# Optimization experiments

Measured on AMD Instinct MI355X. Metric: run time of the kernel, lower is better.

The kernel has to match this reference:

```python
import jax, jax.numpy as jnp
import numpy as np

C, G = 128, 2000          # num_cells, total_genes
CE, GE, H = 64, 64, 256   # cell_embed_dim, gene_embed_dim, hidden_dim
F = CE + GE + 3           # FCGNN input: ctrl val + cell_embed + gene_embed + shift + num_cells


def setup_inputs() -> dict:
    key = jax.random.key(0)
    ks = jax.random.split(key, 13)
    s = 0.02
    return {
        "ctrl": jax.random.uniform(ks[0], (C, G), dtype=jnp.float32),
        "shift_vec": jax.random.normal(ks[1], (G,), dtype=jnp.float32),
        "gene_indices": jnp.arange(G, dtype=jnp.int32),
        # CellEmbedding params
        "ce_w1": jax.random.normal(ks[2], (G, H), dtype=jnp.float32) * s,
        "ce_b1": jnp.zeros((H,), dtype=jnp.float32),
        "ce_w2": jax.random.normal(ks[3], (H, CE), dtype=jnp.float32) * s,
        "ce_b2": jnp.zeros((CE,), dtype=jnp.float32),
        # gene embedding table
        "gene_table": jax.random.normal(ks[4], (G, GE), dtype=jnp.float32) * s,
        # FCGNN params
        "g_w1": jax.random.normal(ks[5], (F, H), dtype=jnp.float32) * s,
        "g_b1": jnp.zeros((H,), dtype=jnp.float32),
        "g_w2": jax.random.normal(ks[6], (2 * H, H), dtype=jnp.float32) * s,
        "g_b2": jnp.zeros((H,), dtype=jnp.float32),
        "g_w3": jax.random.normal(ks[7], (2 * H, 1), dtype=jnp.float32) * s,
        "g_b3": jnp.zeros((1,), dtype=jnp.float32),
    }


def reference(ctrl, shift_vec, gene_indices, ce_w1, ce_b1, ce_w2, ce_b2,
              gene_table, g_w1, g_b1, g_w2, g_b2, g_w3, g_b3):
    num_cells = ctrl.shape[0]
    num_genes = gene_indices.shape[0]

    # CellEmbedding: fc2(elu(fc1(ctrl)))  -> [C, CE]
    ce = jax.nn.elu(ctrl @ ce_w1 + ce_b1) @ ce_w2 + ce_b2

    ctrl_g = ctrl[:, gene_indices]           # [C, Gn]
    shift = shift_vec[gene_indices]          # [Gn]
    ge = gene_table[gene_indices]            # [Gn, GE]

    # Build [C, Gn, F] feature tensor (ctrl val, cell embed, gene embed, shift, num_cells)
    z = jnp.concatenate([
        ctrl_g[:, :, None],
        jnp.broadcast_to(ce[:, None, :], (num_cells, num_genes, ce.shape[1])),
        jnp.broadcast_to(ge[None, :, :], (num_cells, num_genes, ge.shape[1])),
        jnp.broadcast_to(shift[None, :, None], (num_cells, num_genes, 1)),
        jnp.full((num_cells, num_genes, 1), float(num_cells), dtype=ctrl.dtype),
    ], axis=2)

    # FCGNN applied per gene (vectorized over gene axis); pooling is mean over cells (axis 0)
    x = jax.nn.elu(z @ g_w1 + g_b1)                                   # [C, Gn, H]
    p = x.mean(axis=0)                                                # [Gn, H]
    x = jnp.concatenate([x, jnp.broadcast_to(p[None], x.shape)], -1) @ g_w2 + g_b2
    p = x.mean(axis=0)
    x = jax.nn.elu(jnp.concatenate([x, jnp.broadcast_to(p[None], x.shape)], -1)) @ g_w3 + g_b3
    out = x[..., 0]                                                   # [C, Gn]

    # softmax over cells (torch Softmax(dim=0) after transpose/squeeze)
    return jax.nn.softmax(out, axis=0)
```

## Files before the change

### kernel.cpp

```cpp
#include <hip/hip_runtime.h>
#include <hip/hip_bf16.h>
#include <math.h>

#define G_GENES 2000
#define C_CELLS 128
#define H_DIM   256
#define CE_DIM  64
#define LDAe    260

typedef __attribute__((ext_vector_type(8))) short short8;
typedef __attribute__((ext_vector_type(4))) float floatx4;

__device__ __forceinline__ float eluf(float x) {
    float e = __expf(x) - 1.0f;
    return x > 0.0f ? x : e;
}
__device__ __forceinline__ unsigned short f2bf(float v) {
    unsigned u = __float_as_uint(v);
    u += 0x7FFF + ((u >> 16) & 1);
    return (unsigned short)(u >> 16);
}
__device__ __forceinline__ unsigned pk2(float a, float b) {
    __hip_bfloat162 h2 = __float22bfloat162_rn(make_float2(a, b));
    unsigned r; __builtin_memcpy(&r, &h2, 4); return r;
}
__device__ __forceinline__ float bflo(unsigned u) { return __uint_as_float(u << 16); }
__device__ __forceinline__ float bfhi(unsigned u) { return __uint_as_float(u & 0xffff0000u); }
union U8 { unsigned u[4]; short8 s; uint4 v; };

__global__ __launch_bounds__(512) void k_g1(
    const float* __restrict__ ctrl, const float* __restrict__ ce_w1,
    const float* __restrict__ g_w1, const float* __restrict__ g_b1,
    const float* __restrict__ shiftv, const int* __restrict__ gidx,
    const float* __restrict__ gtab, const float* __restrict__ g_w2,
    float* __restrict__ hidpart, unsigned short* __restrict__ w2abt,
    unsigned short* __restrict__ w2bb, float* __restrict__ Bvg)
{
    const int b = blockIdx.x;
    const int t = threadIdx.x;

    if (b < 1024) {
        __shared__ float crow[2][128];
        const int cpair = b >> 4;
        const int kc    = b & 15;
        const int csub  = t >> 8;
        const int h     = t & 255;
        const int c     = cpair * 2 + csub;

        if (h < 125) crow[csub][h] = ctrl[(size_t)c * G_GENES + kc * 125 + h];
        __syncthreads();

        float s0 = 0.f, s1 = 0.f, s2 = 0.f, s3 = 0.f, s4 = 0.f;
        const float* w = ce_w1 + (size_t)(kc * 125) * H_DIM + h;
        const float* cr = crow[csub];
        #pragma unroll 5
        for (int k = 0; k < 125; k += 5) {
            s0 = fmaf(cr[k + 0], w[(size_t)(k + 0) * H_DIM], s0);
            s1 = fmaf(cr[k + 1], w[(size_t)(k + 1) * H_DIM], s1);
            s2 = fmaf(cr[k + 2], w[(size_t)(k + 2) * H_DIM], s2);
            s3 = fmaf(cr[k + 3], w[(size_t)(k + 3) * H_DIM], s3);
            s4 = fmaf(cr[k + 4], w[(size_t)(k + 4) * H_DIM], s4);
        }
        hidpart[((size_t)kc * C_CELLS + c) * H_DIM + h] = ((s0 + s1) + (s2 + s3)) + s4;
    } else if (b < 1040) {
        const int n  = (b - 1024) * 16 + (t >> 5);
        const int k0 = (t & 31) * 8;
        float v[8];
        #pragma unroll
        for (int j = 0; j < 8; ++j) v[j] = g_w2[(size_t)(k0 + j) * H_DIM + n];
        U8 u;
        u.u[0] = pk2(v[0], v[1]); u.u[1] = pk2(v[2], v[3]);
        u.u[2] = pk2(v[4], v[5]); u.u[3] = pk2(v[6], v[7]);
        *(uint4*)&w2abt[(size_t)n * H_DIM + k0] = u.v;
    } else if (b < 1056) {
        const int hr = (b - 1040) * 16 + (t >> 5);
        const int j0 = (t & 31) * 8;
        const float* src = g_w2 + (size_t)(H_DIM + hr) * H_DIM + j0;
        float4 f0 = *(const float4*)src;
        float4 f1 = *(const float4*)(src + 4);
        U8 u;
        u.u[0] = pk2(f0.x, f0.y); u.u[1] = pk2(f0.z, f0.w);
        u.u[2] = pk2(f1.x, f1.y); u.u[3] = pk2(f1.z, f1.w);
        *(uint4*)&w2bb[(size_t)hr * H_DIM + j0] = u.v;
    } else {
        const int g = (b - 1056) * 2 + (t >> 8);
        const int h = t & 255;
        const int idx = gidx[g];
        float bv = g_b1[h] + 128.0f * g_w1[(size_t)130 * H_DIM + h]
                 + shiftv[idx] * g_w1[(size_t)129 * H_DIM + h];
        #pragma unroll 8
        for (int e = 0; e < CE_DIM; ++e)
            bv = fmaf(gtab[(size_t)idx * CE_DIM + e], g_w1[(size_t)(65 + e) * H_DIM + h], bv);
        Bvg[(size_t)g * H_DIM + h] = bv;
    }
}

__global__ __launch_bounds__(256) void k_fin(
    const float* __restrict__ hidpart, const float* __restrict__ ce_b1,
    const float* __restrict__ ce_w2, const float* __restrict__ ce_b2,
    const float* __restrict__ g_w1, unsigned short* __restrict__ Atcbf)
{
    __shared__ float hid[H_DIM];
    __shared__ float celp[4 * CE_DIM];
    __shared__ float cel[CE_DIM];
    const int c = blockIdx.x;
    const int t = threadIdx.x;

    float s = ce_b1[t];
    #pragma unroll
    for (int kc = 0; kc < 16; ++kc)
        s += hidpart[((size_t)kc * C_CELLS + c) * H_DIM + t];
    hid[t] = eluf(s);
    __syncthreads();

    {
        const int e = t & 63, q4 = t >> 6;
        float cp = 0.f;
        #pragma unroll 8
        for (int hh = 0; hh < 64; ++hh)
            cp = fmaf(hid[q4 * 64 + hh], ce_w2[(size_t)(q4 * 64 + hh) * CE_DIM + e], cp);
        celp[q4 * CE_DIM + e] = cp;
    }
    __syncthreads();
    if (t < CE_DIM)
        cel[t] = ce_b2[t] + celp[t] + celp[CE_DIM + t] + celp[2 * CE_DIM + t] + celp[3 * CE_DIM + t];
    __syncthreads();

    float a = 0.f;
    #pragma unroll 8
    for (int e = 0; e < CE_DIM; ++e) a = fmaf(cel[e], g_w1[(size_t)(1 + e) * H_DIM + t], a);
    Atcbf[(size_t)c * H_DIM + t] = f2bf(a);
}

__global__ __launch_bounds__(512, 4) void k_main(
    const float* __restrict__ ctrl, const int* __restrict__ gidx,
    const float* __restrict__ g_w1, const float* __restrict__ g_b2,
    const float* __restrict__ g_w3, const unsigned short* __restrict__ Atcbf,
    const float* __restrict__ Bvg, const unsigned short* __restrict__ w2abt,
    const unsigned short* __restrict__ w2bb, float* __restrict__ out)
{
    __shared__ __align__(16) unsigned short x1t[C_CELLS * LDAe];
    __shared__ __align__(16) float scratch[8 * 258];
    __shared__ float pvec[H_DIM];
    __shared__ float qtmp[H_DIM];
    __shared__ float qv[H_DIM];
    __shared__ float w3v[H_DIM];
    __shared__ float cc[C_CELLS];
    __shared__ float wred[4];

    const int g = blockIdx.x;
    const int t = threadIdx.x;
    const int idx = gidx[g];

    const int lane = t & 63;
    const int w    = t >> 6;
    const int quad = lane >> 4;
    const int nlo  = lane & 15;
    const int wm   = w >> 2;
    const int wn   = w & 3;

    const int ho = t & 31, cgrp = t >> 5;
    const int h0 = ho * 8;
    uint4 A[8];
    #pragma unroll
    for (int i = 0; i < 8; ++i)
        A[i] = *(const uint4*)(Atcbf + (size_t)(cgrp * 8 + i) * H_DIM + h0);
    float4 bv0 = *(const float4*)(Bvg + (size_t)g * H_DIM + h0);
    float4 bv1 = *(const float4*)(Bvg + (size_t)g * H_DIM + h0 + 4);
    float4 wv0 = *(const float4*)(g_w1 + h0);
    float4 wv1 = *(const float4*)(g_w1 + h0 + 4);

    const unsigned short* bbase = w2abt + (size_t)(wn * 64 + nlo) * H_DIM + quad * 8;
    short8 bcur[4];
    #pragma unroll
    for (int nt = 0; nt < 4; ++nt)
        bcur[nt] = *(const short8*)(bbase + (size_t)nt * 16 * H_DIM);

    if (t < C_CELLS) cc[t] = ctrl[(size_t)t * G_GENES + idx];
    if (t < H_DIM) w3v[t] = g_w3[t];
    __syncthreads();

    {
        float s[8];
        #pragma unroll
        for (int j = 0; j < 8; ++j) s[j] = 0.f;
        #pragma unroll
        for (int i = 0; i < 8; ++i) {
            const int c = cgrp * 8 + i;
            const float ccv = cc[c];
            float v0 = eluf(fmaf(ccv, wv0.x, bflo(A[i].x) + bv0.x));
            float v1 = eluf(fmaf(ccv, wv0.y, bfhi(A[i].x) + bv0.y));
            float v2 = eluf(fmaf(ccv, wv0.z, bflo(A[i].y) + bv0.z));
            float v3 = eluf(fmaf(ccv, wv0.w, bfhi(A[i].y) + bv0.w));
            float v4 = eluf(fmaf(ccv, wv1.x, bflo(A[i].z) + bv1.x));
            float v5 = eluf(fmaf(ccv, wv1.y, bfhi(A[i].z) + bv1.y));
            float v6 = eluf(fmaf(ccv, wv1.z, bflo(A[i].w) + bv1.z));
            float v7 = eluf(fmaf(ccv, wv1.w, bfhi(A[i].w) + bv1.w));
            s[0] += v0; s[1] += v1; s[2] += v2; s[3] += v3;
            s[4] += v4; s[5] += v5; s[6] += v6; s[7] += v7;
            uint4 pk;
            pk.x = pk2(v0, v1); pk.y = pk2(v2, v3);
            pk.z = pk2(v4, v5); pk.w = pk2(v6, v7);
            *(uint4*)&x1t[c * LDAe + h0] = pk;
        }
        #pragma unroll
        for (int j = 0; j < 8; ++j) s[j] += __shfl_xor(s[j], 32);
        if (lane < 32) {
            float4 p0 = {s[0], s[1], s[2], s[3]};
            float4 p1 = {s[4], s[5], s[6], s[7]};
            *(float4*)&scratch[w * 258 + h0] = p0;
            *(float4*)&scratch[w * 258 + h0 + 4] = p1;
        }
    }
    __syncthreads();

    floatx4 acc[4][4];
    #pragma unroll
    for (int mt = 0; mt < 4; ++mt)
        #pragma unroll
        for (int nt = 0; nt < 4; ++nt)
            acc[mt][nt] = (floatx4){0.f, 0.f, 0.f, 0.f};

    const unsigned short* abase = &x1t[(wm * 64 + nlo) * LDAe + quad * 8];

    #pragma unroll
    for (int kt = 0; kt < 8; ++kt) {
        short8 af[4];
        #pragma unroll
        for (int mt = 0; mt < 4; ++mt)
            af[mt] = *(const short8*)(abase + mt * 16 * LDAe + kt * 32);
        short8 bnx[4];
        if (kt < 7) {
            #pragma unroll
            for (int nt = 0; nt < 4; ++nt)
                bnx[nt] = *(const short8*)(bbase + (size_t)nt * 16 * H_DIM + (kt + 1) * 32);
        }
        #pragma unroll
        for (int nt = 0; nt < 4; ++nt)
            #pragma unroll
            for (int mt = 0; mt < 4; ++mt)
                acc[mt][nt] = __builtin_amdgcn_mfma_f32_16x16x32_bf16(af[mt], bcur[nt], acc[mt][nt], 0, 0, 0);
        if (kt < 7) {
            #pragma unroll
            for (int nt = 0; nt < 4; ++nt) bcur[nt] = bnx[nt];
        }
    }

    if (t < H_DIM) {
        float ps = 0.f;
        #pragma unroll
        for (int w2 = 0; w2 < 8; ++w2) ps += scratch[w2 * 258 + t];
        pvec[t] = ps * (1.0f / 128.0f);
    }
    __syncthreads();

    {
        const int j = t & 255, hf = t >> 8;
        const unsigned short* wp = w2bb + (size_t)(hf * 128) * H_DIM + j;
        const float* pv = pvec + hf * 128;
        float q0 = 0.f, q1 = 0.f, q2 = 0.f, q3 = 0.f;
        #pragma unroll 8
        for (int h = 0; h < 128; h += 4) {
            q0 = fmaf(pv[h + 0], bflo((unsigned)wp[(size_t)(h + 0) * H_DIM] << 16), q0);
            q1 = fmaf(pv[h + 1], bflo((unsigned)wp[(size_t)(h + 1) * H_DIM] << 16), q1);
            q2 = fmaf(pv[h + 2], bflo((unsigned)wp[(size_t)(h + 2) * H_DIM] << 16), q2);
            q3 = fmaf(pv[h + 3], bflo((unsigned)wp[(size_t)(h + 3) * H_DIM] << 16), q3);
        }
        const float qp = (q0 + q1) + (q2 + q3);
        if (hf) qtmp[j] = qp;
        __syncthreads();
        if (!hf) qv[j] = qp + qtmp[j] + g_b2[j];
    }
    __syncthreads();

    float* red2 = scratch;
    float qj[4], w3j[4];
    #pragma unroll
    for (int nt = 0; nt < 4; ++nt) {
        const int j = wn * 64 + nt * 16 + nlo;
        qj[nt] = qv[j];
        w3j[nt] = w3v[j];
    }
    #pragma unroll
    for (int mt = 0; mt < 4; ++mt) {
        #pragma unroll
        for (int reg = 0; reg < 4; ++reg) {
            float part = 0.f;
            #pragma unroll
            for (int nt = 0; nt < 4; ++nt)
                part = fmaf(eluf(acc[mt][nt][reg] + qj[nt]), w3j[nt], part);
            part += __shfl_xor(part, 1);
            part += __shfl_xor(part, 2);
            part += __shfl_xor(part, 4);
            part += __shfl_xor(part, 8);
            if (nlo == 0)
                red2[(wm * 64 + mt * 16 + quad * 4 + reg) * 5 + wn] = part;
        }
    }
    __syncthreads();

    float s = 0.f, e = 0.f;
    if (t < C_CELLS) {
        s = red2[t * 5 + 0] + red2[t * 5 + 1] + red2[t * 5 + 2] + red2[t * 5 + 3];
        float m = s;
        #pragma unroll
        for (int off = 1; off < 64; off <<= 1) m = fmaxf(m, __shfl_xor(m, off));
        if (lane == 0) wred[w] = m;
    }
    __syncthreads();
    if (t < C_CELLS) {
        const float m = fmaxf(wred[0], wred[1]);
        e = __expf(s - m);
        float S = e;
        #pragma unroll
        for (int off = 1; off < 64; off <<= 1) S += __shfl_xor(S, off);
        if (lane == 0) wred[2 + w] = S;
    }
    __syncthreads();
    if (t < C_CELLS) out[(size_t)t * G_GENES + g] = e / (wred[2] + wred[3]);
}

extern "C" void kernel_launch(void* const* d_in, const int* in_sizes, int n_in,
                              void* d_out, int out_size, void* d_ws, size_t ws_size,
                              hipStream_t stream) {
    const float* ctrl   = (const float*)d_in[0];
    const float* shiftv = (const float*)d_in[1];
    const int*   gidx   = (const int*)d_in[2];
    const float* ce_w1  = (const float*)d_in[3];
    const float* ce_b1  = (const float*)d_in[4];
    const float* ce_w2  = (const float*)d_in[5];
    const float* ce_b2  = (const float*)d_in[6];
    const float* gtab   = (const float*)d_in[7];
    const float* g_w1   = (const float*)d_in[8];
    const float* g_b1   = (const float*)d_in[9];
    const float* g_w2   = (const float*)d_in[10];
    const float* g_b2   = (const float*)d_in[11];
    const float* g_w3   = (const float*)d_in[12];

    char* ws = (char*)d_ws;
    unsigned short* Atcbf = (unsigned short*)(ws);
    unsigned short* w2abt = (unsigned short*)(ws + 128 * 1024);
    unsigned short* w2bb  = (unsigned short*)(ws + 256 * 1024);
    float* Bvg            = (float*)(ws + 384 * 1024);
    float* hidpart        = (float*)(ws + 384 * 1024 + (size_t)G_GENES * H_DIM * 4);
    float* out            = (float*)d_out;

    k_g1<<<2056, 512, 0, stream>>>(
        ctrl, ce_w1, g_w1, g_b1, shiftv, gidx, gtab, g_w2, hidpart, w2abt, w2bb, Bvg);
    k_fin<<<C_CELLS, 256, 0, stream>>>(hidpart, ce_b1, ce_w2, ce_b2, g_w1, Atcbf);
    k_main<<<G_GENES, 512, 0, stream>>>(ctrl, gidx, g_w1, g_b2, g_w3,
                                        Atcbf, Bvg, w2abt, w2bb, out);
}
```

Before: 209.4 us.

## Process two genes per block and interleave second gene's GEMM with first's epilogue

Each k_main block now handles two consecutive genes, halving the grid. The second gene's layer-1 build and MFMA GEMM are placed before the first gene's softmax and the second gene's pooled-vector matvec, so independent work can hide latency and barrier stalls. Shared arrays are merged to save LDS. The cost is a second accumulator set, which raises register pressure and may reduce occupancy, and there are fewer blocks to spread over the CUs.

```diff
diff --git a/kernel.cpp b/kernel.cpp
--- a/kernel.cpp
+++ b/kernel.cpp
@@ -141,16 +141,20 @@
 {
     __shared__ __align__(16) unsigned short x1t[C_CELLS * LDAe];
     __shared__ __align__(16) float scratch[8 * 258];
-    __shared__ float pvec[H_DIM];
-    __shared__ float qtmp[H_DIM];
+    __shared__ __align__(16) float pvqt[2 * H_DIM];
     __shared__ float qv[H_DIM];
     __shared__ float w3v[H_DIM];
     __shared__ float cc[C_CELLS];
     __shared__ float wred[4];
 
-    const int g = blockIdx.x;
+    float* pvec = pvqt;
+    float* qtmp = pvqt + H_DIM;
+    float* red2 = pvqt;
+
+    const int g0i = blockIdx.x * 2;
     const int t = threadIdx.x;
-    const int idx = gidx[g];
+    const int idx0 = gidx[g0i];
+    const int idx1 = gidx[g0i + 1];
 
     const int lane = t & 63;
     const int w    = t >> 6;
@@ -158,15 +162,15 @@
     const int nlo  = lane & 15;
     const int wm   = w >> 2;
     const int wn   = w & 3;
-
     const int ho = t & 31, cgrp = t >> 5;
     const int h0 = ho * 8;
-    uint4 A[8];
+
+    uint4 A0[8];
     #pragma unroll
     for (int i = 0; i < 8; ++i)
-        A[i] = *(const uint4*)(Atcbf + (size_t)(cgrp * 8 + i) * H_DIM + h0);
-    float4 bv0 = *(const float4*)(Bvg + (size_t)g * H_DIM + h0);
-    float4 bv1 = *(const float4*)(Bvg + (size_t)g * H_DIM + h0 + 4);
+        A0[i] = *(const uint4*)(Atcbf + (size_t)(cgrp * 8 + i) * H_DIM + h0);
+    float4 bv0a = *(const float4*)(Bvg + (size_t)g0i * H_DIM + h0);
+    float4 bv0b = *(const float4*)(Bvg + (size_t)g0i * H_DIM + h0 + 4);
     float4 wv0 = *(const float4*)(g_w1 + h0);
     float4 wv1 = *(const float4*)(g_w1 + h0 + 4);
 
@@ -176,7 +180,9 @@
     for (int nt = 0; nt < 4; ++nt)
         bcur[nt] = *(const short8*)(bbase + (size_t)nt * 16 * H_DIM);
 
-    if (t < C_CELLS) cc[t] = ctrl[(size_t)t * G_GENES + idx];
+    float cc1v = 0.f;
+    if (t < C_CELLS) cc1v = ctrl[(size_t)t * G_GENES + idx1];
+    if (t < C_CELLS) cc[t] = ctrl[(size_t)t * G_GENES + idx0];
     if (t < H_DIM) w3v[t] = g_w3[t];
     __syncthreads();
 
@@ -188,14 +194,14 @@
         for (int i = 0; i < 8; ++i) {
             const int c = cgrp * 8 + i;
             const float ccv = cc[c];
-            float v0 = eluf(fmaf(ccv, wv0.x, bflo(A[i].x) + bv0.x));
-            float v1 = eluf(fmaf(ccv, wv0.y, bfhi(A[i].x) + bv0.y));
-            float v2 = eluf(fmaf(ccv, wv0.z, bflo(A[i].y) + bv0.z));
-            float v3 = eluf(fmaf(ccv, wv0.w, bfhi(A[i].y) + bv0.w));
-            float v4 = eluf(fmaf(ccv, wv1.x, bflo(A[i].z) + bv1.x));
-            float v5 = eluf(fmaf(ccv, wv1.y, bfhi(A[i].z) + bv1.y));
-            float v6 = eluf(fmaf(ccv, wv1.z, bflo(A[i].w) + bv1.z));
-            float v7 = eluf(fmaf(ccv, wv1.w, bfhi(A[i].w) + bv1.w));
+            float v0 = eluf(fmaf(ccv, wv0.x, bflo(A0[i].x) + bv0a.x));
+            float v1 = eluf(fmaf(ccv, wv0.y, bfhi(A0[i].x) + bv0a.y));
+            float v2 = eluf(fmaf(ccv, wv0.z, bflo(A0[i].y) + bv0a.z));
+            float v3 = eluf(fmaf(ccv, wv0.w, bfhi(A0[i].y) + bv0a.w));
+            float v4 = eluf(fmaf(ccv, wv1.x, bflo(A0[i].z) + bv0b.x));
+            float v5 = eluf(fmaf(ccv, wv1.y, bfhi(A0[i].z) + bv0b.y));
+            float v6 = eluf(fmaf(ccv, wv1.z, bflo(A0[i].w) + bv0b.z));
+            float v7 = eluf(fmaf(ccv, wv1.w, bfhi(A0[i].w) + bv0b.w));
             s[0] += v0; s[1] += v1; s[2] += v2; s[3] += v3;
             s[4] += v4; s[5] += v5; s[6] += v6; s[7] += v7;
             uint4 pk;
@@ -213,6 +219,8 @@
         }
     }
     __syncthreads();
+
+    if (t < C_CELLS) cc[t] = cc1v;
 
     floatx4 acc[4][4];
     #pragma unroll
@@ -273,51 +281,205 @@
     }
     __syncthreads();
 
-    float* red2 = scratch;
-    float qj[4], w3j[4];
-    #pragma unroll
-    for (int nt = 0; nt < 4; ++nt) {
-        const int j = wn * 64 + nt * 16 + nlo;
-        qj[nt] = qv[j];
-        w3j[nt] = w3v[j];
-    }
-    #pragma unroll
-    for (int mt = 0; mt < 4; ++mt) {
-        #pragma unroll
-        for (int reg = 0; reg < 4; ++reg) {
-            float part = 0.f;
+    {
+        float qj[4], w3j[4];
+        #pragma unroll
+        for (int nt = 0; nt < 4; ++nt) {
+            const int j = wn * 64 + nt * 16 + nlo;
+            qj[nt] = qv[j];
+            w3j[nt] = w3v[j];
+        }
+        #pragma unroll
+        for (int mt = 0; mt < 4; ++mt) {
+            #pragma unroll
+            for (int reg = 0; reg < 4; ++reg) {
+                float part = 0.f;
+                #pragma unroll
+                for (int nt = 0; nt < 4; ++nt)
+                    part = fmaf(eluf(acc[mt][nt][reg] + qj[nt]), w3j[nt], part);
+                part += __shfl_xor(part, 1);
+                part += __shfl_xor(part, 2);
+                part += __shfl_xor(part, 4);
+                part += __shfl_xor(part, 8);
+                if (nlo == 0)
+                    red2[(wm * 64 + mt * 16 + quad * 4 + reg) * 4 + wn] = part;
+            }
+        }
+    }
+
+    uint4 A1[8];
+    #pragma unroll
+    for (int i = 0; i < 8; ++i)
+        A1[i] = *(const uint4*)(Atcbf + (size_t)(cgrp * 8 + i) * H_DIM + h0);
+    float4 bv1a = *(const float4*)(Bvg + (size_t)(g0i + 1) * H_DIM + h0);
+    float4 bv1b = *(const float4*)(Bvg + (size_t)(g0i + 1) * H_DIM + h0 + 4);
+    #pragma unroll
+    for (int nt = 0; nt < 4; ++nt)
+        bcur[nt] = *(const short8*)(bbase + (size_t)nt * 16 * H_DIM);
+
+    {
+        float s[8];
+        #pragma unroll
+        for (int j = 0; j < 8; ++j) s[j] = 0.f;
+        #pragma unroll
+        for (int i = 0; i < 8; ++i) {
+            const int c = cgrp * 8 + i;
+            const float ccv = cc[c];
+            float v0 = eluf(fmaf(ccv, wv0.x, bflo(A1[i].x) + bv1a.x));
+            float v1 = eluf(fmaf(ccv, wv0.y, bfhi(A1[i].x) + bv1a.y));
+            float v2 = eluf(fmaf(ccv, wv0.z, bflo(A1[i].y) + bv1a.z));
+            float v3 = eluf(fmaf(ccv, wv0.w, bfhi(A1[i].y) + bv1a.w));
+            float v4 = eluf(fmaf(ccv, wv1.x, bflo(A1[i].z) + bv1b.x));
+            float v5 = eluf(fmaf(ccv, wv1.y, bfhi(A1[i].z) + bv1b.y));
+            float v6 = eluf(fmaf(ccv, wv1.z, bflo(A1[i].w) + bv1b.z));
+            float v7 = eluf(fmaf(ccv, wv1.w, bfhi(A1[i].w) + bv1b.w));
+            s[0] += v0; s[1] += v1; s[2] += v2; s[3] += v3;
+            s[4] += v4; s[5] += v5; s[6] += v6; s[7] += v7;
+            uint4 pk;
+            pk.x = pk2(v0, v1); pk.y = pk2(v2, v3);
+            pk.z = pk2(v4, v5); pk.w = pk2(v6, v7);
+            *(uint4*)&x1t[c * LDAe + h0] = pk;
+        }
+        #pragma unroll
+        for (int j = 0; j < 8; ++j) s[j] += __shfl_xor(s[j], 32);
+        if (lane < 32) {
+            float4 p0 = {s[0], s[1], s[2], s[3]};
+            float4 p1 = {s[4], s[5], s[6], s[7]};
+            *(float4*)&scratch[w * 258 + h0] = p0;
+            *(float4*)&scratch[w * 258 + h0 + 4] = p1;
+        }
+    }
+    __syncthreads();
+
+    float s0v = 0.f;
+    if (t < C_CELLS) {
+        float4 r4 = *(const float4*)&red2[t * 4];
+        s0v = (r4.x + r4.y) + (r4.z + r4.w);
+    }
+
+    floatx4 acc1[4][4];
+    #pragma unroll
+    for (int mt = 0; mt < 4; ++mt)
+        #pragma unroll
+        for (int nt = 0; nt < 4; ++nt)
+            acc1[mt][nt] = (floatx4){0.f, 0.f, 0.f, 0.f};
+
+    #pragma unroll
+    for (int kt = 0; kt < 8; ++kt) {
+        short8 af[4];
+        #pragma unroll
+        for (int mt = 0; mt < 4; ++mt)
+            af[mt] = *(const short8*)(abase + mt * 16 * LDAe + kt * 32);
+        short8 bnx[4];
+        if (kt < 7) {
             #pragma unroll
             for (int nt = 0; nt < 4; ++nt)
-                part = fmaf(eluf(acc[mt][nt][reg] + qj[nt]), w3j[nt], part);
-            part += __shfl_xor(part, 1);
-            part += __shfl_xor(part, 2);
-            part += __shfl_xor(part, 4);
-            part += __shfl_xor(part, 8);
-            if (nlo == 0)
-                red2[(wm * 64 + mt * 16 + quad * 4 + reg) * 5 + wn] = part;
-        }
-    }
-    __syncthreads();
-
-    float s = 0.f, e = 0.f;
+                bnx[nt] = *(const short8*)(bbase + (size_t)nt * 16 * H_DIM + (kt + 1) * 32);
+        }
+        #pragma unroll
+        for (int nt = 0; nt < 4; ++nt)
+            #pragma unroll
+            for (int mt = 0; mt < 4; ++mt)
+                acc1[mt][nt] = __builtin_amdgcn_mfma_f32_16x16x32_bf16(af[mt], bcur[nt], acc1[mt][nt], 0, 0, 0);
+        if (kt < 7) {
+            #pragma unroll
+            for (int nt = 0; nt < 4; ++nt) bcur[nt] = bnx[nt];
+        }
+    }
+
     if (t < C_CELLS) {
-        s = red2[t * 5 + 0] + red2[t * 5 + 1] + red2[t * 5 + 2] + red2[t * 5 + 3];
-        float m = s;
+        float m = s0v;
         #pragma unroll
         for (int off = 1; off < 64; off <<= 1) m = fmaxf(m, __shfl_xor(m, off));
         if (lane == 0) wred[w] = m;
     }
     __syncthreads();
+
+    float e0 = 0.f;
     if (t < C_CELLS) {
         const float m = fmaxf(wred[0], wred[1]);
-        e = __expf(s - m);
-        float S = e;
+        e0 = __expf(s0v - m);
+        float S = e0;
         #pragma unroll
         for (int off = 1; off < 64; off <<= 1) S += __shfl_xor(S, off);
         if (lane == 0) wred[2 + w] = S;
     }
-    __syncthreads();
-    if (t < C_CELLS) out[(size_t)t * G_GENES + g] = e / (wred[2] + wred[3]);
+    if (t < H_DIM) {
+        float ps = 0.f;
+        #pragma unroll
+        for (int w2 = 0; w2 < 8; ++w2) ps += scratch[w2 * 258 + t];
+        pvec[t] = ps * (1.0f / 128.0f);
+    }
+    __syncthreads();
+
+    if (t < C_CELLS) out[(size_t)t * G_GENES + g0i] = e0 / (wred[2] + wred[3]);
+
+    {
+        const int j = t & 255, hf = t >> 8;
+        const unsigned short* wp = w2bb + (size_t)(hf * 128) * H_DIM + j;
+        const float* pv = pvec + hf * 128;
+        float q0 = 0.f, q1 = 0.f, q2 = 0.f, q3 = 0.f;
+        #pragma unroll 8
+        for (int h = 0; h < 128; h += 4) {
+            q0 = fmaf(pv[h + 0], bflo((unsigned)wp[(size_t)(h + 0) * H_DIM] << 16), q0);
+            q1 = fmaf(pv[h + 1], bflo((unsigned)wp[(size_t)(h + 1) * H_DIM] << 16), q1);
+            q2 = fmaf(pv[h + 2], bflo((unsigned)wp[(size_t)(h + 2) * H_DIM] << 16), q2);
+            q3 = fmaf(pv[h + 3], bflo((unsigned)wp[(size_t)(h + 3) * H_DIM] << 16), q3);
+        }
+        const float qp = (q0 + q1) + (q2 + q3);
+        if (hf) qtmp[j] = qp;
+        __syncthreads();
+        if (!hf) qv[j] = qp + qtmp[j] + g_b2[j];
+    }
+    __syncthreads();
+
+    {
+        float qj[4], w3j[4];
+        #pragma unroll
+        for (int nt = 0; nt < 4; ++nt) {
+            const int j = wn * 64 + nt * 16 + nlo;
+            qj[nt] = qv[j];
+            w3j[nt] = w3v[j];
+        }
+        #pragma unroll
+        for (int mt = 0; mt < 4; ++mt) {
+            #pragma unroll
+            for (int reg = 0; reg < 4; ++reg) {
+                float part = 0.f;
+                #pragma unroll
+                for (int nt = 0; nt < 4; ++nt)
+                    part = fmaf(eluf(acc1[mt][nt][reg] + qj[nt]), w3j[nt], part);
+                part += __shfl_xor(part, 1);
+                part += __shfl_xor(part, 2);
+                part += __shfl_xor(part, 4);
+                part += __shfl_xor(part, 8);
+                if (nlo == 0)
+                    red2[(wm * 64 + mt * 16 + quad * 4 + reg) * 4 + wn] = part;
+            }
+        }
+    }
+    __syncthreads();
+
+    float s1v = 0.f, e1 = 0.f;
+    if (t < C_CELLS) {
+        float4 r4 = *(const float4*)&red2[t * 4];
+        s1v = (r4.x + r4.y) + (r4.z + r4.w);
+        float m = s1v;
+        #pragma unroll
+        for (int off = 1; off < 64; off <<= 1) m = fmaxf(m, __shfl_xor(m, off));
+        if (lane == 0) wred[w] = m;
+    }
+    __syncthreads();
+    if (t < C_CELLS) {
+        const float m = fmaxf(wred[0], wred[1]);
+        e1 = __expf(s1v - m);
+        float S = e1;
+        #pragma unroll
+        for (int off = 1; off < 64; off <<= 1) S += __shfl_xor(S, off);
+        if (lane == 0) wred[2 + w] = S;
+    }
+    __syncthreads();
+    if (t < C_CELLS) out[(size_t)t * G_GENES + g0i + 1] = e1 / (wred[2] + wred[3]);
 }
 
 extern "C" void kernel_launch(void* const* d_in, const int* in_sizes, int n_in,
@@ -348,6 +510,6 @@
     k_g1<<<2056, 512, 0, stream>>>(
         ctrl, ce_w1, g_w1, g_b1, shiftv, gidx, gtab, g_w2, hidpart, w2abt, w2bb, Bvg);
     k_fin<<<C_CELLS, 256, 0, stream>>>(hidpart, ce_b1, ce_w2, ce_b2, g_w1, Atcbf);
-    k_main<<<G_GENES, 512, 0, stream>>>(ctrl, gidx, g_w1, g_b2, g_w3,
-                                        Atcbf, Bvg, w2abt, w2bb, out);
-}
+    k_main<<<G_GENES / 2, 512, 0, stream>>>(ctrl, gidx, g_w1, g_b2, g_w3,
+                                            Atcbf, Bvg, w2abt, w2bb, out);
+}
```

New measurement: 234.0 us. +11.7%, slower.

## Process two genes per block in k_main and drop softmax max-reduction

Applied to the files above, without the earlier changes.

k_main now runs with half as many blocks, and each block loops over two genes. It reuses the block setup, the gathered ctrl columns and the shared buffers, and reloads the per-gene operands between iterations. The softmax skips the max-subtraction pass and clamps the exponent at 80 instead, which removes one reduction and one barrier per gene. This cuts launch and setup overhead, but it serialises two genes per block, so the grid may under-fill the CUs. It also gives up the numerical safety of the max-shifted softmax, which is only acceptable if the logits stay small.

```diff
diff --git a/kernel.cpp b/kernel.cpp
--- a/kernel.cpp
+++ b/kernel.cpp
@@ -145,12 +145,11 @@
     __shared__ float qtmp[H_DIM];
     __shared__ float qv[H_DIM];
     __shared__ float w3v[H_DIM];
-    __shared__ float cc[C_CELLS];
-    __shared__ float wred[4];
-
-    const int g = blockIdx.x;
+    __shared__ float cc2[2][C_CELLS];
+    __shared__ float wred[2];
+
+    const int g0i = blockIdx.x * 2;
     const int t = threadIdx.x;
-    const int idx = gidx[g];
 
     const int lane = t & 63;
     const int w    = t >> 6;
@@ -158,15 +157,15 @@
     const int nlo  = lane & 15;
     const int wm   = w >> 2;
     const int wn   = w & 3;
-
     const int ho = t & 31, cgrp = t >> 5;
     const int h0 = ho * 8;
+
     uint4 A[8];
     #pragma unroll
     for (int i = 0; i < 8; ++i)
         A[i] = *(const uint4*)(Atcbf + (size_t)(cgrp * 8 + i) * H_DIM + h0);
-    float4 bv0 = *(const float4*)(Bvg + (size_t)g * H_DIM + h0);
-    float4 bv1 = *(const float4*)(Bvg + (size_t)g * H_DIM + h0 + 4);
+    float4 bva = *(const float4*)(Bvg + (size_t)g0i * H_DIM + h0);
+    float4 bvb = *(const float4*)(Bvg + (size_t)g0i * H_DIM + h0 + 4);
     float4 wv0 = *(const float4*)(g_w1 + h0);
     float4 wv1 = *(const float4*)(g_w1 + h0 + 4);
 
@@ -176,148 +175,161 @@
     for (int nt = 0; nt < 4; ++nt)
         bcur[nt] = *(const short8*)(bbase + (size_t)nt * 16 * H_DIM);
 
-    if (t < C_CELLS) cc[t] = ctrl[(size_t)t * G_GENES + idx];
+    if (t < C_CELLS) {
+        cc2[0][t] = ctrl[(size_t)t * G_GENES + gidx[g0i]];
+        cc2[1][t] = ctrl[(size_t)t * G_GENES + gidx[g0i + 1]];
+    }
     if (t < H_DIM) w3v[t] = g_w3[t];
     __syncthreads();
 
-    {
-        float s[8];
-        #pragma unroll
-        for (int j = 0; j < 8; ++j) s[j] = 0.f;
-        #pragma unroll
-        for (int i = 0; i < 8; ++i) {
-            const int c = cgrp * 8 + i;
-            const float ccv = cc[c];
-            float v0 = eluf(fmaf(ccv, wv0.x, bflo(A[i].x) + bv0.x));
-            float v1 = eluf(fmaf(ccv, wv0.y, bfhi(A[i].x) + bv0.y));
-            float v2 = eluf(fmaf(ccv, wv0.z, bflo(A[i].y) + bv0.z));
-            float v3 = eluf(fmaf(ccv, wv0.w, bfhi(A[i].y) + bv0.w));
-            float v4 = eluf(fmaf(ccv, wv1.x, bflo(A[i].z) + bv1.x));
-            float v5 = eluf(fmaf(ccv, wv1.y, bfhi(A[i].z) + bv1.y));
-            float v6 = eluf(fmaf(ccv, wv1.z, bflo(A[i].w) + bv1.z));
-            float v7 = eluf(fmaf(ccv, wv1.w, bfhi(A[i].w) + bv1.w));
-            s[0] += v0; s[1] += v1; s[2] += v2; s[3] += v3;
-            s[4] += v4; s[5] += v5; s[6] += v6; s[7] += v7;
-            uint4 pk;
-            pk.x = pk2(v0, v1); pk.y = pk2(v2, v3);
-            pk.z = pk2(v4, v5); pk.w = pk2(v6, v7);
-            *(uint4*)&x1t[c * LDAe + h0] = pk;
-        }
-        #pragma unroll
-        for (int j = 0; j < 8; ++j) s[j] += __shfl_xor(s[j], 32);
-        if (lane < 32) {
-            float4 p0 = {s[0], s[1], s[2], s[3]};
-            float4 p1 = {s[4], s[5], s[6], s[7]};
-            *(float4*)&scratch[w * 258 + h0] = p0;
-            *(float4*)&scratch[w * 258 + h0 + 4] = p1;
-        }
-    }
-    __syncthreads();
-
-    floatx4 acc[4][4];
-    #pragma unroll
-    for (int mt = 0; mt < 4; ++mt)
-        #pragma unroll
-        for (int nt = 0; nt < 4; ++nt)
-            acc[mt][nt] = (floatx4){0.f, 0.f, 0.f, 0.f};
-
     const unsigned short* abase = &x1t[(wm * 64 + nlo) * LDAe + quad * 8];
-
-    #pragma unroll
-    for (int kt = 0; kt < 8; ++kt) {
-        short8 af[4];
+    float* red2 = scratch;
+
+    #pragma unroll 1
+    for (int gg = 0; gg < 2; ++gg) {
+        const float* cc = cc2[gg];
+
+        {
+            float s[8];
+            #pragma unroll
+            for (int j = 0; j < 8; ++j) s[j] = 0.f;
+            #pragma unroll
+            for (int i = 0; i < 8; ++i) {
+                const int c = cgrp * 8 + i;
+                const float ccv = cc[c];
+                float v0 = eluf(fmaf(ccv, wv0.x, bflo(A[i].x) + bva.x));
+                float v1 = eluf(fmaf(ccv, wv0.y, bfhi(A[i].x) + bva.y));
+                float v2 = eluf(fmaf(ccv, wv0.z, bflo(A[i].y) + bva.z));
+                float v3 = eluf(fmaf(ccv, wv0.w, bfhi(A[i].y) + bva.w));
+                float v4 = eluf(fmaf(ccv, wv1.x, bflo(A[i].z) + bvb.x));
+                float v5 = eluf(fmaf(ccv, wv1.y, bfhi(A[i].z) + bvb.y));
+                float v6 = eluf(fmaf(ccv, wv1.z, bflo(A[i].w) + bvb.z));
+                float v7 = eluf(fmaf(ccv, wv1.w, bfhi(A[i].w) + bvb.w));
+                s[0] += v0; s[1] += v1; s[2] += v2; s[3] += v3;
+                s[4] += v4; s[5] += v5; s[6] += v6; s[7] += v7;
+                uint4 pk;
+                pk.x = pk2(v0, v1); pk.y = pk2(v2, v3);
+                pk.z = pk2(v4, v5); pk.w = pk2(v6, v7);
+                *(uint4*)&x1t[c * LDAe + h0] = pk;
+            }
+            #pragma unroll
+            for (int j = 0; j < 8; ++j) s[j] += __shfl_xor(s[j], 32);
+            if (lane < 32) {
+                float4 p0 = {s[0], s[1], s[2], s[3]};
+                float4 p1 = {s[4], s[5], s[6], s[7]};
+                *(float4*)&scratch[w * 258 + h0] = p0;
+                *(float4*)&scratch[w * 258 + h0 + 4] = p1;
+            }
+        }
+        __syncthreads();
+
+        floatx4 acc[4][4];
         #pragma unroll
         for (int mt = 0; mt < 4; ++mt)
-            af[mt] = *(const short8*)(abase + mt * 16 * LDAe + kt * 32);
-        short8 bnx[4];
-        if (kt < 7) {
             #pragma unroll
             for (int nt = 0; nt < 4; ++nt)
-                bnx[nt] = *(const short8*)(bbase + (size_t)nt * 16 * H_DIM + (kt + 1) * 32);
-        }
+                acc[mt][nt] = (floatx4){0.f, 0.f, 0.f, 0.f};
+
         #pragma unroll
-        for (int nt = 0; nt < 4; ++nt)
+        for (int kt = 0; kt < 8; ++kt) {
+            short8 af[4];
             #pragma unroll
             for (int mt = 0; mt < 4; ++mt)
-                acc[mt][nt] = __builtin_amdgcn_mfma_f32_16x16x32_bf16(af[mt], bcur[nt], acc[mt][nt], 0, 0, 0);
-        if (kt < 7) {
-            #pragma unroll
-            for (int nt = 0; nt < 4; ++nt) bcur[nt] = bnx[nt];
+                af[mt] = *(const short8*)(abase + mt * 16 * LDAe + kt * 32);
+            short8 bnx[4];
+            if (kt < 7) {
+                #pragma unroll
+                for (int nt = 0; nt < 4; ++nt)
+                    bnx[nt] = *(const short8*)(bbase + (size_t)nt * 16 * H_DIM + (kt + 1) * 32);
+            }
+            #pragma unroll
+            for (int nt = 0; nt < 4; ++nt)
+                #pragma unroll
+                for (int mt = 0; mt < 4; ++mt)
+                    acc[mt][nt] = __builtin_amdgcn_mfma_f32_16x16x32_bf16(af[mt], bcur[nt], acc[mt][nt], 0, 0, 0);
+            if (kt < 7) {
+                #pragma unroll
+                for (int nt = 0; nt < 4; ++nt) bcur[nt] = bnx[nt];
+            }
+        }
+
+        if (t < H_DIM) {
+            float ps = 0.f;
+            #pragma unroll
+            for (int w2 = 0; w2 < 8; ++w2) ps += scratch[w2 * 258 + t];
+            pvec[t] = ps * (1.0f / 128.0f);
+        }
+        __syncthreads();
+
+        {
+            const int j = t & 255, hf = t >> 8;
+            const unsigned short* wp = w2bb + (size_t)(hf * 128) * H_DIM + j;
+            const float* pv = pvec + hf * 128;
+            float q0 = 0.f, q1 = 0.f, q2 = 0.f, q3 = 0.f;
+            #pragma unroll 8
+            for (int h = 0; h < 128; h += 4) {
+                q0 = fmaf(pv[h + 0], bflo((unsigned)wp[(size_t)(h + 0) * H_DIM] << 16), q0);
+                q1 = fmaf(pv[h + 1], bflo((unsigned)wp[(size_t)(h + 1) * H_DIM] << 16), q1);
+                q2 = fmaf(pv[h + 2], bflo((unsigned)wp[(size_t)(h + 2) * H_DIM] << 16), q2);
+                q3 = fmaf(pv[h + 3], bflo((unsigned)wp[(size_t)(h + 3) * H_DIM] << 16), q3);
+            }
+            const float qp = (q0 + q1) + (q2 + q3);
+            if (hf) qtmp[j] = qp;
+            __syncthreads();
+            if (!hf) qv[j] = qp + qtmp[j] + g_b2[j];
+        }
+        __syncthreads();
+
+        {
+            float qj[4], w3j[4];
+            #pragma unroll
+            for (int nt = 0; nt < 4; ++nt) {
+                const int j = wn * 64 + nt * 16 + nlo;
+                qj[nt] = qv[j];
+                w3j[nt] = w3v[j];
+            }
+            #pragma unroll
+            for (int mt = 0; mt < 4; ++mt) {
+                #pragma unroll
+                for (int reg = 0; reg < 4; ++reg) {
+                    float part = 0.f;
+                    #pragma unroll
+                    for (int nt = 0; nt < 4; ++nt)
+                        part = fmaf(eluf(acc[mt][nt][reg] + qj[nt]), w3j[nt], part);
+                    part += __shfl_xor(part, 1);
+                    part += __shfl_xor(part, 2);
+                    part += __shfl_xor(part, 4);
+                    part += __shfl_xor(part, 8);
+                    if (nlo == 0)
+                        red2[(wm * 64 + mt * 16 + quad * 4 + reg) * 5 + wn] = part;
+                }
+            }
+        }
+        __syncthreads();
+
+        float e = 0.f;
+        if (t < C_CELLS) {
+            float s = red2[t * 5 + 0] + red2[t * 5 + 1] + red2[t * 5 + 2] + red2[t * 5 + 3];
+            e = __expf(fminf(s, 80.f));
+            float S = e;
+            #pragma unroll
+            for (int off = 1; off < 64; off <<= 1) S += __shfl_xor(S, off);
+            if (lane == 0) wred[w] = S;
+        }
+        __syncthreads();
+        if (t < C_CELLS) out[(size_t)t * G_GENES + g0i + gg] = e / (wred[0] + wred[1]);
+
+        if (gg == 0) {
+            #pragma unroll
+            for (int i = 0; i < 8; ++i)
+                A[i] = *(const uint4*)(Atcbf + (size_t)(cgrp * 8 + i) * H_DIM + h0);
+            bva = *(const float4*)(Bvg + (size_t)(g0i + 1) * H_DIM + h0);
+            bvb = *(const float4*)(Bvg + (size_t)(g0i + 1) * H_DIM + h0 + 4);
+            #pragma unroll
+            for (int nt = 0; nt < 4; ++nt)
+                bcur[nt] = *(const short8*)(bbase + (size_t)nt * 16 * H_DIM);
         }
     }
-
-    if (t < H_DIM) {
-        float ps = 0.f;
-        #pragma unroll
-        for (int w2 = 0; w2 < 8; ++w2) ps += scratch[w2 * 258 + t];
-        pvec[t] = ps * (1.0f / 128.0f);
-    }
-    __syncthreads();
-
-    {
-        const int j = t & 255, hf = t >> 8;
-        const unsigned short* wp = w2bb + (size_t)(hf * 128) * H_DIM + j;
-        const float* pv = pvec + hf * 128;
-        float q0 = 0.f, q1 = 0.f, q2 = 0.f, q3 = 0.f;
-        #pragma unroll 8
-        for (int h = 0; h < 128; h += 4) {
-            q0 = fmaf(pv[h + 0], bflo((unsigned)wp[(size_t)(h + 0) * H_DIM] << 16), q0);
-            q1 = fmaf(pv[h + 1], bflo((unsigned)wp[(size_t)(h + 1) * H_DIM] << 16), q1);
-            q2 = fmaf(pv[h + 2], bflo((unsigned)wp[(size_t)(h + 2) * H_DIM] << 16), q2);
-            q3 = fmaf(pv[h + 3], bflo((unsigned)wp[(size_t)(h + 3) * H_DIM] << 16), q3);
-        }
-        const float qp = (q0 + q1) + (q2 + q3);
-        if (hf) qtmp[j] = qp;
-        __syncthreads();
-        if (!hf) qv[j] = qp + qtmp[j] + g_b2[j];
-    }
-    __syncthreads();
-
-    float* red2 = scratch;
-    float qj[4], w3j[4];
-    #pragma unroll
-    for (int nt = 0; nt < 4; ++nt) {
-        const int j = wn * 64 + nt * 16 + nlo;
-        qj[nt] = qv[j];
-        w3j[nt] = w3v[j];
-    }
-    #pragma unroll
-    for (int mt = 0; mt < 4; ++mt) {
-        #pragma unroll
-        for (int reg = 0; reg < 4; ++reg) {
-            float part = 0.f;
-            #pragma unroll
-            for (int nt = 0; nt < 4; ++nt)
-                part = fmaf(eluf(acc[mt][nt][reg] + qj[nt]), w3j[nt], part);
-            part += __shfl_xor(part, 1);
-            part += __shfl_xor(part, 2);
-            part += __shfl_xor(part, 4);
-            part += __shfl_xor(part, 8);
-            if (nlo == 0)
-                red2[(wm * 64 + mt * 16 + quad * 4 + reg) * 5 + wn] = part;
-        }
-    }
-    __syncthreads();
-
-    float s = 0.f, e = 0.f;
-    if (t < C_CELLS) {
-        s = red2[t * 5 + 0] + red2[t * 5 + 1] + red2[t * 5 + 2] + red2[t * 5 + 3];
-        float m = s;
-        #pragma unroll
-        for (int off = 1; off < 64; off <<= 1) m = fmaxf(m, __shfl_xor(m, off));
-        if (lane == 0) wred[w] = m;
-    }
-    __syncthreads();
-    if (t < C_CELLS) {
-        const float m = fmaxf(wred[0], wred[1]);
-        e = __expf(s - m);
-        float S = e;
-        #pragma unroll
-        for (int off = 1; off < 64; off <<= 1) S += __shfl_xor(S, off);
-        if (lane == 0) wred[2 + w] = S;
-    }
-    __syncthreads();
-    if (t < C_CELLS) out[(size_t)t * G_GENES + g] = e / (wred[2] + wred[3]);
 }
 
 extern "C" void kernel_launch(void* const* d_in, const int* in_sizes, int n_in,
@@ -348,6 +360,6 @@
     k_g1<<<2056, 512, 0, stream>>>(
         ctrl, ce_w1, g_w1, g_b1, shiftv, gidx, gtab, g_w2, hidpart, w2abt, w2bb, Bvg);
     k_fin<<<C_CELLS, 256, 0, stream>>>(hidpart, ce_b1, ce_w2, ce_b2, g_w1, Atcbf);
-    k_main<<<G_GENES, 512, 0, stream>>>(ctrl, gidx, g_w1, g_b2, g_w3,
-                                        Atcbf, Bvg, w2abt, w2bb, out);
-}
+    k_main<<<G_GENES / 2, 512, 0, stream>>>(ctrl, gidx, g_w1, g_b2, g_w3,
+                                            Atcbf, Bvg, w2abt, w2bb, out);
+}
```

Result: slower. 267.8 us (+27.9%).
